# Kernel tuning notes

Hardware: AMD Instinct MI355X
Metric: run time of the kernel (lower is better)

The kernel has to match this reference:

```python
import jax, jax.numpy as jnp
import numpy as np

N_NODES = 50000
N_EDGES = 1000000
D = 64


def _seg_sum(vals, idx, n):
    return jax.ops.segment_sum(vals, idx, num_segments=n)


def gcn_conv(x, row, col, ew, W, b):
    """PyG GCNConv with edge_weight: self-loops (w=1), symmetric norm, aggr=add."""
    n = x.shape[0]
    loop = jnp.arange(n, dtype=row.dtype)
    row_a = jnp.concatenate([row, loop])
    col_a = jnp.concatenate([col, loop])
    w_a = jnp.concatenate([ew, jnp.ones((n,), dtype=ew.dtype)])
    deg = _seg_sum(w_a, col_a, n)                      # weighted in-degree at target
    dinv = jnp.where(deg > 0, deg ** -0.5, 0.0)
    norm = dinv[row_a] * w_a * dinv[col_a]             # [E+N]
    xw = x @ W                                          # [N, out]
    msg = norm[:, None] * xw[row_a]                    # gather + scale
    return _seg_sum(msg, col_a, n) + b                 # scatter-add + bias


def hetero_conv(x, row, col, ew, W, b):
    """message = ew * Linear(|x_i - x_j|); aggr=add at target (col)."""
    n = x.shape[0]
    diff = jnp.abs(x[col] - x[row])                    # [E, in]
    msg = ew[:, None] * (diff @ W + b)                 # gate scales bias too
    return _seg_sum(msg, col, n)


def setup_inputs() -> dict:
    key = jax.random.key(0)
    ks = jax.random.split(key, 8)
    s = 1.0 / np.sqrt(D)
    x = jax.random.normal(ks[0], (N_NODES, D), dtype=jnp.float32)
    edge_index = jax.random.randint(ks[1], (2, N_EDGES), 0, N_NODES, dtype=jnp.int32)
    edge_curvature = jax.random.normal(ks[2], (N_EDGES,), dtype=jnp.float32)
    return {
        "x": x,
        "edge_index": edge_index,
        "edge_curvature": edge_curvature,
        "W_homo1": jax.random.normal(ks[3], (D, D), jnp.float32) * s,
        "b_homo1": jnp.zeros((D,), jnp.float32),
        "W_homo2": jax.random.normal(ks[4], (D, D), jnp.float32) * s,
        "b_homo2": jnp.zeros((D,), jnp.float32),
        "W_het1": jax.random.normal(ks[5], (D, D), jnp.float32) * s,
        "b_het1": jax.random.normal(ks[6], (D,), jnp.float32) * s,
        "W_het2": jax.random.normal(ks[7], (D, D), jnp.float32) * s,
        "b_het2": jnp.zeros((D,), jnp.float32),
    }


def reference(x, edge_index, edge_curvature,
              W_homo1, b_homo1, W_homo2, b_homo2,
              W_het1, b_het1, W_het2, b_het2):
    row, col = edge_index[0], edge_index[1]
    gate = jax.nn.sigmoid(edge_curvature / 5.0)        # [E]
    g_homo, g_het = gate, 1.0 - gate
    # layer 1
    h = gcn_conv(x, row, col, g_homo, W_homo1, b_homo1) \
        + hetero_conv(x, row, col, g_het, W_het1, b_het1)
    h = jax.nn.relu(h)                                  # dropout = identity (eval)
    # layer 2 (no activation)
    out = gcn_conv(h, row, col, g_homo, W_homo2, b_homo2) \
        + hetero_conv(h, row, col, g_het, W_het2, b_het2)
    return out
```

## Files before the change

### kernel.cpp

```cpp
#include <hip/hip_runtime.h>
#include <math.h>


#define D 64
#define PSHIFT 45
#define PSCALE 274877906944.0f
#define PMASK  ((1ull << PSHIFT) - 1)

typedef unsigned long long u64;
typedef int iv4 __attribute__((ext_vector_type(4)));

__global__ void k_phase1(const int* __restrict__ col, const float* __restrict__ curv,
                         u64* __restrict__ packed, float* __restrict__ gbuf,
                         unsigned short* __restrict__ rank, int E) {
  int e = blockIdx.x * blockDim.x + threadIdx.x;
  if (e >= E) return;
  int c = col[e];
  float g = 1.0f / (1.0f + expf(-curv[e] * 0.2f));
  gbuf[e] = g;
  u64 inc = ((u64)1 << PSHIFT) | (u64)(g * PSCALE);
  u64 old = atomicAdd(&packed[c], inc);
  rank[e] = (unsigned short)(old >> PSHIFT);
}

__global__ void k_scanA(const u64* __restrict__ packed, int* __restrict__ part,
                        int* __restrict__ bsum, int n) {
  __shared__ int tmp[256];
  int tid = threadIdx.x;
  int gid = blockIdx.x * 256 + tid;
  int v = (gid < n) ? (int)(packed[gid] >> PSHIFT) : 0;
  tmp[tid] = v;
  __syncthreads();
  for (int off = 1; off < 256; off <<= 1) {
    int t = (tid >= off) ? tmp[tid - off] : 0;
    __syncthreads();
    tmp[tid] += t;
    __syncthreads();
  }
  if (gid < n) part[gid] = tmp[tid] - v;
  if (tid == 255) bsum[blockIdx.x] = tmp[255];
}

__global__ void k_scanB(int* __restrict__ bsum, int nb) {
  __shared__ int tmp[256];
  int tid = threadIdx.x;
  int v = (tid < nb) ? bsum[tid] : 0;
  tmp[tid] = v;
  __syncthreads();
  for (int off = 1; off < 256; off <<= 1) {
    int t = (tid >= off) ? tmp[tid - off] : 0;
    __syncthreads();
    tmp[tid] += t;
    __syncthreads();
  }
  if (tid < nb) bsum[tid] = tmp[tid] - v;
}

__global__ void k_scanC(const int* __restrict__ part, const int* __restrict__ bsum,
                        const u64* __restrict__ packed,
                        int* __restrict__ ptr, float* __restrict__ dinv,
                        int n, int E) {
  int gid = blockIdx.x * 256 + threadIdx.x;
  if (gid < n) {
    ptr[gid] = part[gid] + bsum[gid >> 8];
    float degw = (float)(packed[gid] & PMASK) * (1.0f / PSCALE);
    dinv[gid] = rsqrtf(1.0f + degw);
  }
  if (gid == 0) ptr[n] = E;
}

__global__ void k_fill(const int* __restrict__ row, const int* __restrict__ col,
                       const float* __restrict__ gbuf,
                       const unsigned short* __restrict__ rank,
                       const int* __restrict__ ptr, const float* __restrict__ dinv,
                       iv4* __restrict__ meta, int E) {
  int e = blockIdx.x * blockDim.x + threadIdx.x;
  if (e >= E) return;
  int c = col[e];
  int r = row[e];
  float g = gbuf[e];
  int pos = ptr[c] + rank[e];
  iv4 m;
  m.x = r;
  m.y = __float_as_int(dinv[r] * g * dinv[c]);
  m.z = __float_as_int(1.0f - g);
  m.w = 0;
  meta[pos] = m;
}

__global__ __launch_bounds__(256) void k_agg(
    const float* __restrict__ v, const int* __restrict__ ptr,
    const iv4* __restrict__ meta, const float* __restrict__ dinv,
    float* __restrict__ aggG, float* __restrict__ aggS,
    float* __restrict__ swv, int n) {
  int wid = __builtin_amdgcn_readfirstlane(threadIdx.x >> 6);
  int lane = threadIdx.x & 63;
  int c = blockIdx.x * 4 + wid;
  if (c >= n) return;

  float vc = v[(size_t)c * D + lane];
  float dc = dinv[c];
  float accG = dc * dc * vc;
  float accS = 0.0f, sw = 0.0f;
  int s = ptr[c], e = ptr[c + 1];

  int i = s;
#pragma unroll 1
  for (; i + 8 <= e; i += 8) {
    iv4 m[8];
    float vr[8];
#pragma unroll
    for (int u = 0; u < 8; ++u) m[u] = __builtin_nontemporal_load(&meta[i + u]);
#pragma unroll
    for (int u = 0; u < 8; ++u) vr[u] = v[(size_t)m[u].x * D + lane];
#pragma unroll
    for (int u = 0; u < 8; ++u) {
      float nrm = __int_as_float(m[u].y);
      float gh  = __int_as_float(m[u].z);
      accG = fmaf(nrm, vr[u], accG);
      accS = fmaf(gh, fabsf(vc - vr[u]), accS);
      sw += gh;
    }
  }
  for (; i < e; ++i) {
    iv4 m = __builtin_nontemporal_load(&meta[i]);
    float vr = v[(size_t)m.x * D + lane];
    float nrm = __int_as_float(m.y);
    float gh  = __int_as_float(m.z);
    accG = fmaf(nrm, vr, accG);
    accS = fmaf(gh, fabsf(vc - vr), accS);
    sw += gh;
  }

  aggG[(size_t)c * D + lane] = accG;
  aggS[(size_t)c * D + lane] = accS;
  if (lane == 0) swv[c] = sw;
}

#define AP4 17
#define FMA4(i, j)                                         \
  acc[i][0] = fmaf(a4[i].j, w4j.x, acc[i][0]);             \
  acc[i][1] = fmaf(a4[i].j, w4j.y, acc[i][1]);             \
  acc[i][2] = fmaf(a4[i].j, w4j.z, acc[i][2]);             \
  acc[i][3] = fmaf(a4[i].j, w4j.w, acc[i][3]);

__global__ __launch_bounds__(256) void k_mlp(
    const float* __restrict__ aggG, const float* __restrict__ aggS,
    const float* __restrict__ swv,
    const float* __restrict__ Wh, const float* __restrict__ bh,
    const float* __restrict__ Wt, const float* __restrict__ bt,
    float* __restrict__ out, int n, int do_relu) {
  __shared__ float As[64 * 68];
  __shared__ float Ws[64 * 64];
  int tid = threadIdx.x;
  int tx = tid & 15, ty = tid >> 4;
  int base = blockIdx.x * 64;

  float acc[4][4] = {{0.f}};
  const float* aggX = aggG;
  const float* Wx = Wh;

  for (int half = 0; half < 2; ++half) {
#pragma unroll
    for (int j = 0; j < 4; ++j) {
      int idx = tid + j * 256;
      ((float4*)Ws)[idx] = ((const float4*)Wx)[idx];
    }
#pragma unroll
    for (int j = 0; j < 4; ++j) {
      int idx = tid + j * 256;
      int nl = idx >> 4, kk = idx & 15;
      int gn = min(base + nl, n - 1);
      ((float4*)As)[nl * AP4 + kk] = ((const float4*)aggX)[(size_t)gn * 16 + kk];
    }
    __syncthreads();

#pragma unroll
    for (int kk4 = 0; kk4 < 16; ++kk4) {
      float4 a4[4];
#pragma unroll
      for (int i = 0; i < 4; ++i)
        a4[i] = ((const float4*)As)[(4 * ty + i) * AP4 + kk4];
      {
        float4 w4j = ((const float4*)Ws)[(kk4 * 4 + 0) * 16 + tx];
        FMA4(0, x) FMA4(1, x) FMA4(2, x) FMA4(3, x)
      }
      {
        float4 w4j = ((const float4*)Ws)[(kk4 * 4 + 1) * 16 + tx];
        FMA4(0, y) FMA4(1, y) FMA4(2, y) FMA4(3, y)
      }
      {
        float4 w4j = ((const float4*)Ws)[(kk4 * 4 + 2) * 16 + tx];
        FMA4(0, z) FMA4(1, z) FMA4(2, z) FMA4(3, z)
      }
      {
        float4 w4j = ((const float4*)Ws)[(kk4 * 4 + 3) * 16 + tx];
        FMA4(0, w) FMA4(1, w) FMA4(2, w) FMA4(3, w)
      }
    }
    __syncthreads();
    aggX = aggS;
    Wx = Wt;
  }

  float4 bh4 = ((const float4*)bh)[tx];
  float4 bt4 = ((const float4*)bt)[tx];
#pragma unroll
  for (int i = 0; i < 4; ++i) {
    int node = base + 4 * ty + i;
    if (node < n) {
      float s = swv[node];
      float4 r;
      r.x = fmaf(s, bt4.x, acc[i][0] + bh4.x);
      r.y = fmaf(s, bt4.y, acc[i][1] + bh4.y);
      r.z = fmaf(s, bt4.z, acc[i][2] + bh4.z);
      r.w = fmaf(s, bt4.w, acc[i][3] + bh4.w);
      if (do_relu) {
        r.x = fmaxf(r.x, 0.f); r.y = fmaxf(r.y, 0.f);
        r.z = fmaxf(r.z, 0.f); r.w = fmaxf(r.w, 0.f);
      }
      ((float4*)out)[(size_t)node * 16 + tx] = r;
    }
  }
}

extern "C" void kernel_launch(void* const* d_in, const int* in_sizes, int n_in,
                              void* d_out, int out_size, void* d_ws, size_t ws_size,
                              hipStream_t stream) {
  const float* x    = (const float*)d_in[0];
  const int*   ei   = (const int*)d_in[1];
  const float* curv = (const float*)d_in[2];
  const float* Wh1  = (const float*)d_in[3];
  const float* bh1  = (const float*)d_in[4];
  const float* Wh2  = (const float*)d_in[5];
  const float* bh2  = (const float*)d_in[6];
  const float* Wt1  = (const float*)d_in[7];
  const float* bt1  = (const float*)d_in[8];
  const float* Wt2  = (const float*)d_in[9];
  const float* bt2  = (const float*)d_in[10];

  int n = in_sizes[0] / D;
  int E = in_sizes[2];
  const int* row = ei;
  const int* col = ei + E;
  float* out = (float*)d_out;

  char* w = (char*)d_ws;
  auto carve = [&](size_t bytes) {
    char* p = w;
    w += (bytes + 255) & ~(size_t)255;
    return (void*)p;
  };
  u64*   packed = (u64*)carve((size_t)n * 8);
  float* dinv   = (float*)carve((size_t)n * 4);
  int*   part   = (int*)carve((size_t)n * 4);
  int*   ptr    = (int*)carve((size_t)(n + 1) * 4);
  int*   bsum   = (int*)carve(256 * 4);
  float* gbuf   = (float*)carve((size_t)E * 4);
  unsigned short* rank = (unsigned short*)carve((size_t)E * 2);
  iv4*   meta   = (iv4*)carve((size_t)E * 16);
  float* h      = (float*)carve((size_t)n * D * 4);
  float* aggG   = (float*)carve((size_t)n * D * 4);
  float* aggS   = (float*)carve((size_t)n * D * 4);
  float* swv    = (float*)carve((size_t)n * 4);

  int nbN = (n + 255) / 256;
  int nbE = (E + 255) / 256;
  int nbA = (n + 3) / 4;
  int nbM = (n + 63) / 64;

  (void)hipMemsetAsync(packed, 0, (size_t)n * 8, stream);
  k_phase1<<<nbE, 256, 0, stream>>>(col, curv, packed, gbuf, rank, E);
  k_scanA<<<nbN, 256, 0, stream>>>(packed, part, bsum, n);
  k_scanB<<<1, 256, 0, stream>>>(bsum, nbN);
  k_scanC<<<nbN, 256, 0, stream>>>(part, bsum, packed, ptr, dinv, n, E);
  k_fill<<<nbE, 256, 0, stream>>>(row, col, gbuf, rank, ptr, dinv, meta, E);

  k_agg<<<nbA, 256, 0, stream>>>(x, ptr, meta, dinv, aggG, aggS, swv, n);
  k_mlp<<<nbM, 256, 0, stream>>>(aggG, aggS, swv, Wh1, bh1, Wt1, bt1, h, n, 1);
  k_agg<<<nbA, 256, 0, stream>>>(h, ptr, meta, dinv, aggG, aggS, swv, n);
  k_mlp<<<nbM, 256, 0, stream>>>(aggG, aggS, swv, Wh2, bh2, Wt2, bt2, out, n, 0);
}
```

Measured before the change: 271.4 us.

## Store node features and edge metadata in fp16 to halve gather traffic

Converts input features and the layer-1 hidden output to fp16, and packs per-edge norm and hetero gate into a half2, shrinking edge metadata from 16 to 8 bytes. The aggregation kernel gathers fp16 neighbour rows and accumulates in fp32. This targets memory bandwidth in the random-gather aggregation, which dominates runtime. It adds a conversion kernel and costs precision on features and edge weights, which may push results past tolerance.

```diff
diff --git a/kernel.cpp b/kernel.cpp
--- a/kernel.cpp
+++ b/kernel.cpp
@@ -1,4 +1,5 @@
 #include <hip/hip_runtime.h>
+#include <hip/hip_fp16.h>
 #include <math.h>
 
 
@@ -8,7 +9,12 @@
 #define PMASK  ((1ull << PSHIFT) - 1)
 
 typedef unsigned long long u64;
-typedef int iv4 __attribute__((ext_vector_type(4)));
+typedef int iv2 __attribute__((ext_vector_type(2)));
+
+__device__ inline float2 h2f2(int bits) {
+  __half2 h = __builtin_bit_cast(__half2, bits);
+  return __half22float2(h);
+}
 
 __global__ void k_phase1(const int* __restrict__ col, const float* __restrict__ curv,
                          u64* __restrict__ packed, float* __restrict__ gbuf,
@@ -23,6 +29,18 @@
   rank[e] = (unsigned short)(old >> PSHIFT);
 }
 
+__global__ void k_cvt(const float* __restrict__ x, __half* __restrict__ xh, int n4) {
+  int i = blockIdx.x * blockDim.x + threadIdx.x;
+  if (i >= n4) return;
+  float4 a = ((const float4*)x)[i];
+  __half2 lo = __floats2half2_rn(a.x, a.y);
+  __half2 hi = __floats2half2_rn(a.z, a.w);
+  iv2 pk;
+  pk.x = __builtin_bit_cast(int, lo);
+  pk.y = __builtin_bit_cast(int, hi);
+  ((iv2*)xh)[i] = pk;
+}
+
 __global__ void k_scanA(const u64* __restrict__ packed, int* __restrict__ part,
                         int* __restrict__ bsum, int n) {
   __shared__ int tmp[256];
@@ -73,24 +91,23 @@
                        const float* __restrict__ gbuf,
                        const unsigned short* __restrict__ rank,
                        const int* __restrict__ ptr, const float* __restrict__ dinv,
-                       iv4* __restrict__ meta, int E) {
+                       iv2* __restrict__ meta, int E) {
   int e = blockIdx.x * blockDim.x + threadIdx.x;
   if (e >= E) return;
   int c = col[e];
   int r = row[e];
   float g = gbuf[e];
   int pos = ptr[c] + rank[e];
-  iv4 m;
+  __half2 ng = __floats2half2_rn(dinv[r] * g * dinv[c], 1.0f - g);
+  iv2 m;
   m.x = r;
-  m.y = __float_as_int(dinv[r] * g * dinv[c]);
-  m.z = __float_as_int(1.0f - g);
-  m.w = 0;
-  meta[pos] = m;
+  m.y = __builtin_bit_cast(int, ng);
+  __builtin_nontemporal_store(m, &meta[pos]);
 }
 
 __global__ __launch_bounds__(256) void k_agg(
-    const float* __restrict__ v, const int* __restrict__ ptr,
-    const iv4* __restrict__ meta, const float* __restrict__ dinv,
+    const __half* __restrict__ v, const int* __restrict__ ptr,
+    const iv2* __restrict__ meta, const float* __restrict__ dinv,
     float* __restrict__ aggG, float* __restrict__ aggS,
     float* __restrict__ swv, int n) {
   int wid = __builtin_amdgcn_readfirstlane(threadIdx.x >> 6);
@@ -98,7 +115,7 @@
   int c = blockIdx.x * 4 + wid;
   if (c >= n) return;
 
-  float vc = v[(size_t)c * D + lane];
+  float vc = __half2float(v[(size_t)c * D + lane]);
   float dc = dinv[c];
   float accG = dc * dc * vc;
   float accS = 0.0f, sw = 0.0f;
@@ -107,29 +124,28 @@
   int i = s;
 #pragma unroll 1
   for (; i + 8 <= e; i += 8) {
-    iv4 m[8];
+    iv2 m[8];
     float vr[8];
 #pragma unroll
     for (int u = 0; u < 8; ++u) m[u] = __builtin_nontemporal_load(&meta[i + u]);
 #pragma unroll
-    for (int u = 0; u < 8; ++u) vr[u] = v[(size_t)m[u].x * D + lane];
+    for (int u = 0; u < 8; ++u)
+      vr[u] = __half2float(v[(size_t)m[u].x * D + lane]);
 #pragma unroll
     for (int u = 0; u < 8; ++u) {
-      float nrm = __int_as_float(m[u].y);
-      float gh  = __int_as_float(m[u].z);
-      accG = fmaf(nrm, vr[u], accG);
-      accS = fmaf(gh, fabsf(vc - vr[u]), accS);
-      sw += gh;
+      float2 ng = h2f2(m[u].y);
+      accG = fmaf(ng.x, vr[u], accG);
+      accS = fmaf(ng.y, fabsf(vc - vr[u]), accS);
+      sw += ng.y;
     }
   }
   for (; i < e; ++i) {
-    iv4 m = __builtin_nontemporal_load(&meta[i]);
-    float vr = v[(size_t)m.x * D + lane];
-    float nrm = __int_as_float(m.y);
-    float gh  = __int_as_float(m.z);
-    accG = fmaf(nrm, vr, accG);
-    accS = fmaf(gh, fabsf(vc - vr), accS);
-    sw += gh;
+    iv2 m = __builtin_nontemporal_load(&meta[i]);
+    float vr = __half2float(v[(size_t)m.x * D + lane]);
+    float2 ng = h2f2(m.y);
+    accG = fmaf(ng.x, vr, accG);
+    accS = fmaf(ng.y, fabsf(vc - vr), accS);
+    sw += ng.y;
   }
 
   aggG[(size_t)c * D + lane] = accG;
@@ -149,7 +165,7 @@
     const float* __restrict__ swv,
     const float* __restrict__ Wh, const float* __restrict__ bh,
     const float* __restrict__ Wt, const float* __restrict__ bt,
-    float* __restrict__ out, int n, int do_relu) {
+    float* __restrict__ out, __half* __restrict__ out_h, int n, int do_relu) {
   __shared__ float As[64 * 68];
   __shared__ float Ws[64 * 64];
   int tid = threadIdx.x;
@@ -219,7 +235,16 @@
         r.x = fmaxf(r.x, 0.f); r.y = fmaxf(r.y, 0.f);
         r.z = fmaxf(r.z, 0.f); r.w = fmaxf(r.w, 0.f);
       }
-      ((float4*)out)[(size_t)node * 16 + tx] = r;
+      if (out_h) {
+        __half2 lo = __floats2half2_rn(r.x, r.y);
+        __half2 hi = __floats2half2_rn(r.z, r.w);
+        iv2 pk;
+        pk.x = __builtin_bit_cast(int, lo);
+        pk.y = __builtin_bit_cast(int, hi);
+        ((iv2*)out_h)[(size_t)node * 16 + tx] = pk;
+      } else {
+        ((float4*)out)[(size_t)node * 16 + tx] = r;
+      }
     }
   }
 }
@@ -258,8 +283,9 @@
   int*   bsum   = (int*)carve(256 * 4);
   float* gbuf   = (float*)carve((size_t)E * 4);
   unsigned short* rank = (unsigned short*)carve((size_t)E * 2);
-  iv4*   meta   = (iv4*)carve((size_t)E * 16);
-  float* h      = (float*)carve((size_t)n * D * 4);
+  iv2*   meta   = (iv2*)carve((size_t)E * 8);
+  __half* xh    = (__half*)carve((size_t)n * D * 2);
+  __half* hh    = (__half*)carve((size_t)n * D * 2);
   float* aggG   = (float*)carve((size_t)n * D * 4);
   float* aggS   = (float*)carve((size_t)n * D * 4);
   float* swv    = (float*)carve((size_t)n * 4);
@@ -268,16 +294,20 @@
   int nbE = (E + 255) / 256;
   int nbA = (n + 3) / 4;
   int nbM = (n + 63) / 64;
+  int n4  = n * D / 4;
 
   (void)hipMemsetAsync(packed, 0, (size_t)n * 8, stream);
   k_phase1<<<nbE, 256, 0, stream>>>(col, curv, packed, gbuf, rank, E);
+  k_cvt<<<(n4 + 255) / 256, 256, 0, stream>>>(x, xh, n4);
   k_scanA<<<nbN, 256, 0, stream>>>(packed, part, bsum, n);
   k_scanB<<<1, 256, 0, stream>>>(bsum, nbN);
   k_scanC<<<nbN, 256, 0, stream>>>(part, bsum, packed, ptr, dinv, n, E);
   k_fill<<<nbE, 256, 0, stream>>>(row, col, gbuf, rank, ptr, dinv, meta, E);
 
-  k_agg<<<nbA, 256, 0, stream>>>(x, ptr, meta, dinv, aggG, aggS, swv, n);
-  k_mlp<<<nbM, 256, 0, stream>>>(aggG, aggS, swv, Wh1, bh1, Wt1, bt1, h, n, 1);
-  k_agg<<<nbA, 256, 0, stream>>>(h, ptr, meta, dinv, aggG, aggS, swv, n);
-  k_mlp<<<nbM, 256, 0, stream>>>(aggG, aggS, swv, Wh2, bh2, Wt2, bt2, out, n, 0);
-}
+  k_agg<<<nbA, 256, 0, stream>>>(xh, ptr, meta, dinv, aggG, aggS, swv, n);
+  k_mlp<<<nbM, 256, 0, stream>>>(aggG, aggS, swv, Wh1, bh1, Wt1, bt1,
+                                 nullptr, hh, n, 1);
+  k_agg<<<nbA, 256, 0, stream>>>(hh, ptr, meta, dinv, aggG, aggS, swv, n);
+  k_mlp<<<nbM, 256, 0, stream>>>(aggG, aggS, swv, Wh2, bh2, Wt2, bt2,
+                                 out, nullptr, n, 0);
+}
```

New measurement: 273.0 us. Within noise of the previous version (+0.6%).
